# Kernel tuning notes

Hardware: AMD Instinct MI355X
Metric: run time of the kernel (lower is better)

Reference implementation:

```python
import jax, jax.numpy as jnp
import numpy as np

SIM_RADIUS = 4
SIM_STRIDE = 1
IN_STRIDES = (8, 16, 32)
REL_STRIDES = tuple(IN_STRIDES[-1] // s for s in IN_STRIDES)  # (4, 2, 1)
BN_EPS = 1e-5


def _base_conv(x, w, g, b, m, v):
    # BaseConv(c, c, ksize=1): bias-free 1x1 conv + BatchNorm2d (eval stats) + SiLU
    # x: [N, Cin, H, W], w: [Cout, Cin]
    y = jnp.einsum('nchw,dc->ndhw', x, w)
    scale = g * jax.lax.rsqrt(v + BN_EPS)
    y = y * scale[None, :, None, None] + (b - m * scale)[None, :, None, None]
    return y * jax.nn.sigmoid(y)


def _interp_indices(pci, fci):
    # Exact port of interpolate_features index selection (tiny, host-side ints).
    pci = np.asarray(pci).astype(np.int64).tolist()
    fci = np.asarray(fci).astype(np.int64).tolist()
    TP = len(pci[0])
    idx = []
    for i, (p, f) in enumerate(zip(pci, fci)):
        p_pos = TP - 2
        for f_i in f:
            while p_pos >= 0:
                if p_pos == 0 or f_i < -p[p_pos - 1]:
                    idx.append(p_pos + i * TP)
                    break
                p_pos -= 1
    return np.asarray(idx, dtype=np.int64)


def _local_corr(f1, f2, radius, step):
    # Full-image correlation over a (2r+1)x(2r+1) grid of shifts with stride `step`.
    # Equivalent to F.conv2d(f1[None], f2[:, None], stride=step, padding=radius*step,
    # groups=N*C). f1, f2: [N, C, H, W] -> [N, C, (2r+1)^2]
    N, C, H, W = f1.shape
    pad = radius * step
    f1p = jnp.pad(f1, ((0, 0), (0, 0), (pad, pad), (pad, pad)))
    sims = []
    for oy in range(2 * radius + 1):
        for ox in range(2 * radius + 1):
            sl = f1p[:, :, oy * step:oy * step + H, ox * step:ox * step + W]
            sims.append(jnp.einsum('nchw,nchw->nc', sl, f2))
    return jnp.stack(sims, axis=-1)


def _forward(feats, conv_params, mlp_w, pci, fci):
    B, TP = pci.shape
    TF = fci.shape[1]
    idx = _interp_indices(pci, fci)  # [B*TF] gather indices into flattened (B*TP)
    sims = []
    for f, (w, g, b, m, v), s in zip(feats, conv_params, REL_STRIDES):
        _, _, C, H, W = f.shape
        pf = _base_conv(f.reshape(B * TP, C, H, W), w, g, b, m, v)  # [B*TP, C, H, W]
        # interpolate_features detaches -> stop_gradient on the gathered clip features
        ipf = jax.lax.stop_gradient(pf[idx])  # [B*TF, C, H, W]
        pf = pf.reshape(B, TP, C, H, W)
        f1 = jnp.broadcast_to(pf[:, -1][:, None], (B, TF, C, H, W)).reshape(B * TF, C, H, W)
        sim = _local_corr(f1, ipf, SIM_RADIUS, SIM_STRIDE * s)  # [B*TF, C, 81]
        sim = jax.nn.softmax(sim, axis=-1)
        sim = jnp.einsum('ncs,s->nc', sim, mlp_w[0])  # Linear(81, 1, bias=False)
        sims.append(sim.reshape(B, TF, C, 1, 1))
    return tuple(sims)


def setup_inputs() -> dict:
    key = jax.random.key(0)
    ks = jax.random.split(key, 20)
    B, TP, TF = 4, 4, 2
    chans = (128, 256, 512)
    hws = ((80, 80), (40, 40), (20, 20))
    d = {}
    for l, (C, (H, W)) in enumerate(zip(chans, hws)):
        d[f'features_{l}'] = jax.random.normal(ks[l], (B, TP, C, H, W), jnp.float32)
        d[f'w{l}'] = jax.random.normal(ks[3 + l], (C, C), jnp.float32) / np.float32(np.sqrt(C))
        d[f'g{l}'] = jnp.ones((C,), jnp.float32)
        d[f'b{l}'] = jnp.zeros((C,), jnp.float32)
        d[f'm{l}'] = 0.1 * jax.random.normal(ks[6 + l], (C,), jnp.float32)
        d[f'v{l}'] = jax.random.uniform(ks[9 + l], (C,), jnp.float32, 0.5, 1.5)
    d['mlp_w'] = jax.random.normal(ks[12], (1, (2 * SIM_RADIUS + 1) ** 2), jnp.float32) / np.float32(2 * SIM_RADIUS + 1)
    d['past_clip_ids'] = jnp.tile(jnp.array([-3, -2, -1, 0], jnp.int32), (B, 1))
    d['future_clip_ids'] = jnp.tile(jnp.array([1, 2], jnp.int32), (B, 1))
    return d


def reference(features_0, features_1, features_2,
              w0, g0, b0, m0, v0,
              w1, g1, b1, m1, v1,
              w2, g2, b2, m2, v2,
              mlp_w, past_clip_ids, future_clip_ids):
    feats = (features_0, features_1, features_2)
    cps = ((w0, g0, b0, m0, v0), (w1, g1, b1, m1, v1), (w2, g2, b2, m2, v2))
    return _forward(feats, cps, mlp_w, np.asarray(past_clip_ids), np.asarray(future_clip_ids))


if __name__ == '__main__':
    outs = reference(**setup_inputs())
    print([o.shape for o in outs])
```

## Files before the change

kernel.cpp:

```cpp
#include <hip/hip_runtime.h>
#include <hip/hip_bf16.h>
#include <math.h>

#define BB 4
#define TPP 4
#define TFF 2
#define NIMG (BB*TPP)
#define NF (BB*TFF)

typedef __attribute__((ext_vector_type(8))) short bf16x8;
typedef __attribute__((ext_vector_type(4))) float f32x4;
#define MFMA16(a,b,c) __builtin_amdgcn_mfma_f32_16x16x32_bf16(a,b,c,0,0,0)

#define GLL(gaddr, laddr) __builtin_amdgcn_global_load_lds( \
    (const __attribute__((address_space(1))) void*)(gaddr), \
    (__attribute__((address_space(3))) void*)(laddr), 16, 0, 0)

__device__ __forceinline__ unsigned short f2bf(float x) {
    __hip_bfloat16 h = __float2bfloat16(x);
    return *reinterpret_cast<unsigned short*>(&h);
}
__device__ __forceinline__ float bf2f(unsigned short u) {
    unsigned int v = ((unsigned int)u) << 16;
    return __uint_as_float(v);
}

__global__ void idx_kernel(const int* __restrict__ pci, const int* __restrict__ fci,
                           int* __restrict__ idx, int* __restrict__ needed)
{
    if (threadIdx.x == 0 && blockIdx.x == 0) {
        for (int n = 0; n < BB*TPP; n++) needed[n] = 0;
        for (int i = 0; i < BB; i++) {
            needed[i*TPP + TPP-1] = 1;
            int p_pos = TPP - 2;
            for (int j = 0; j < TFF; j++) {
                int f = fci[i*TFF + j];
                while (p_pos >= 0) {
                    if (p_pos == 0 || f < -pci[i*TPP + p_pos - 1]) {
                        idx[i*TFF + j] = p_pos + i*TPP;
                        needed[p_pos + i*TPP] = 1;
                        break;
                    }
                    p_pos--;
                }
            }
        }
    }
}

template<int C>
__device__ __forceinline__ void wtile_frag(const float* __restrict__ w,
                                           const float* __restrict__ g,
                                           const float* __restrict__ v,
                                           unsigned short* __restrict__ whi,
                                           unsigned short* __restrict__ wlo, int tile)
{
    constexpr int DT = C/16;
    const int ct = tile / DT, dt = tile % DT;
    const int t = threadIdx.x;
    const size_t base = (size_t)tile * 512;
    #pragma unroll
    for (int e = 0; e < 2; e++) {
        int pos = t*2 + e;
        int lane = pos >> 3, j = pos & 7;
        int m = lane & 15, q = lane >> 4;
        int d = dt*16 + m, c = ct*32 + q*8 + j;
        float sc = g[d] * rsqrtf(v[d] + 1e-5f);
        float x = w[(size_t)d*C + c] * sc;
        unsigned short hi = f2bf(x);
        float lof = x - bf2f(hi);
        whi[base + pos] = hi;
        wlo[base + pos] = f2bf(lof);
    }
}

__global__ __launch_bounds__(256)
void wprep_kernel(const float* w0, const float* g0, const float* b0, const float* m0, const float* v0,
                  unsigned short* whi0, unsigned short* wlo0, float* sh0,
                  const float* w1, const float* g1, const float* b1, const float* m1, const float* v1,
                  unsigned short* whi1, unsigned short* wlo1, float* sh1,
                  const float* w2, const float* g2, const float* b2, const float* m2, const float* v2,
                  unsigned short* whi2, unsigned short* wlo2, float* sh2)
{
    int bid = blockIdx.x;
    if (bid < 32)        wtile_frag<128>(w0, g0, v0, whi0, wlo0, bid);
    else if (bid < 160)  wtile_frag<256>(w1, g1, v1, whi1, wlo1, bid - 32);
    else if (bid < 672)  wtile_frag<512>(w2, g2, v2, whi2, wlo2, bid - 160);
    else {
        for (int i = threadIdx.x; i < 896; i += 256) {
            if (i < 128)      { int d=i;     float sc=g0[d]*rsqrtf(v0[d]+1e-5f); sh0[d]=b0[d]-m0[d]*sc; }
            else if (i < 384) { int d=i-128; float sc=g1[d]*rsqrtf(v1[d]+1e-5f); sh1[d]=b1[d]-m1[d]*sc; }
            else              { int d=i-384; float sc=g2[d]*rsqrtf(v2[d]+1e-5f); sh2[d]=b2[d]-m2[d]*sc; }
        }
    }
}

template<int C, int HW>
__device__ __forceinline__ void conv_mfma_tile(
    const float* __restrict__ x,
    const unsigned short* __restrict__ whi,
    const unsigned short* __restrict__ wlo,
    const float* __restrict__ sh,
    float* __restrict__ pf,
    int n, int dblk, int pblk,
    unsigned short* __restrict__ Ahi, unsigned short* __restrict__ Alo,
    unsigned short* __restrict__ Bhi, unsigned short* __restrict__ Blo)
{
    constexpr int DT = C/16;
    const int tid  = threadIdx.x;
    const int lane = tid & 63;
    const int wv   = tid >> 6;
    const int d0 = dblk*128, p0 = pblk*128;
    const float* xn = x + (size_t)n * C * HW;
    const int wdt = (wv >> 1) * 4;
    const int wpt = (wv & 1) * 4;
    const int kb  = (lane >> 4) * 8;
    const int pn  = lane & 15;

    f32x4 acc[4][4];
    #pragma unroll
    for (int i = 0; i < 4; i++)
        #pragma unroll
        for (int j = 0; j < 4; j++)
            acc[i][j] = f32x4{0.f, 0.f, 0.f, 0.f};

    for (int ct = 0; ct < C/32; ct++) {
        __syncthreads();
        {
            const size_t gb = ((size_t)ct * DT + dblk*8) * 512 + (size_t)lane*8;
            const unsigned short* ghi = whi + gb;
            const unsigned short* glo = wlo + gb;
            GLL(ghi + (size_t)wv*512,     Ahi + wv*512);
            GLL(ghi + (size_t)(wv+4)*512, Ahi + (wv+4)*512);
            GLL(glo + (size_t)wv*512,     Alo + wv*512);
            GLL(glo + (size_t)(wv+4)*512, Alo + (wv+4)*512);
        }
        #pragma unroll
        for (int e = 0; e < 2; e++) {
            int pt = e*4 + (tid >> 6);
            int pp = p0 + pt*16 + pn;
            int pc = pp < HW ? pp : HW-1;
            const float* src = xn + (size_t)(ct*32 + kb) * HW + pc;
            bf16x8 h8, l8;
            #pragma unroll
            for (int j = 0; j < 8; j++) {
                float xv = src[(size_t)j * HW];
                unsigned short hi = f2bf(xv);
                h8[j] = (short)hi;
                l8[j] = (short)f2bf(xv - bf2f(hi));
            }
            int slot = pt*64 + lane;
            *(bf16x8*)(Bhi + slot*8) = h8;
            *(bf16x8*)(Blo + slot*8) = l8;
        }
        __syncthreads();
        bf16x8 bh[4], bl[4];
        #pragma unroll
        for (int j = 0; j < 4; j++) {
            bh[j] = *(const bf16x8*)(Bhi + (wpt+j)*512 + lane*8);
            bl[j] = *(const bf16x8*)(Blo + (wpt+j)*512 + lane*8);
        }
        #pragma unroll
        for (int i = 0; i < 4; i++) {
            bf16x8 ah = *(const bf16x8*)(Ahi + (wdt+i)*512 + lane*8);
            bf16x8 al = *(const bf16x8*)(Alo + (wdt+i)*512 + lane*8);
            #pragma unroll
            for (int j = 0; j < 4; j++) {
                acc[i][j] = MFMA16(ah, bh[j], acc[i][j]);
                acc[i][j] = MFMA16(al, bh[j], acc[i][j]);
                acc[i][j] = MFMA16(ah, bl[j], acc[i][j]);
            }
        }
    }

    const int rowq = (lane >> 4) * 4;
    #pragma unroll
    for (int i = 0; i < 4; i++) {
        #pragma unroll
        for (int r = 0; r < 4; r++) {
            int d = d0 + (wdt+i)*16 + rowq + r;
            float shd = sh[d];
            float* dst = pf + ((size_t)n * C + d) * HW;
            #pragma unroll
            for (int j = 0; j < 4; j++) {
                int p = p0 + (wpt+j)*16 + pn;
                float y = acc[i][j][r] + shd;
                float o = y / (1.f + __expf(-y));
                if (p < HW) dst[p] = o;
            }
        }
    }
}

__global__ __launch_bounds__(256, 2)
void conv_all(const float* x0, const unsigned short* whi0, const unsigned short* wlo0,
              const float* sh0, float* pf0,
              const float* x1, const unsigned short* whi1, const unsigned short* wlo1,
              const float* sh1, float* pf1,
              const float* x2, const unsigned short* whi2, const unsigned short* wlo2,
              const float* sh2, float* pf2,
              const int* __restrict__ needed)
{
    __shared__ __align__(16) unsigned short Ahi[8*512];
    __shared__ __align__(16) unsigned short Alo[8*512];
    __shared__ __align__(16) unsigned short Bhi[8*512];
    __shared__ __align__(16) unsigned short Blo[8*512];
    const int bid = blockIdx.x;
    if (bid < 256) {
        int n = bid >> 4, d = (bid >> 2) & 3, p = bid & 3;
        if (!needed[n]) return;
        conv_mfma_tile<512, 400>(x2, whi2, wlo2, sh2, pf2, n, d, p, Ahi, Alo, Bhi, Blo);
    } else if (bid < 672) {
        int rel = bid - 256;
        int n = rel / 26, rem = rel % 26;
        int d = rem / 13, p = rem % 13;
        if (!needed[n]) return;
        conv_mfma_tile<256, 1600>(x1, whi1, wlo1, sh1, pf1, n, d, p, Ahi, Alo, Bhi, Blo);
    } else {
        int rel = bid - 672;
        int n = rel / 50, p = rel % 50;
        if (!needed[n]) return;
        conv_mfma_tile<128, 6400>(x0, whi0, wlo0, sh0, pf0, n, 0, p, Ahi, Alo, Bhi, Blo);
    }
}

#define MAXPLANE 12544

template<int C, int H, int W, int STEP>
__device__ __forceinline__ void corr_tile(const float* __restrict__ pf,
                                          const int* __restrict__ idx,
                                          const float* __restrict__ mlp,
                                          float* __restrict__ out,
                                          int c, int b, float* __restrict__ smem)
{
    constexpr int PAD  = 4 * STEP;
    constexpr int PW   = W + 2*PAD;
    constexpr int PH   = H + 2*PAD;
    constexpr int HW   = H * W;
    constexpr int QPH   = (HW/4) / 2;
    constexpr int ITERS = (QPH + 63) / 64;
    constexpr int WINF  = 8*STEP + 4;
    constexpr int WIN4  = WINF / 4;

    float* f1s  = smem;
    float* part = smem + MAXPLANE;
    float* simC = part + 324;

    const int tid  = threadIdx.x;
    const int lane = tid & 63;
    const int wave = tid >> 6;
    const int ph   = wave / 3;
    const int kys  = wave % 3;

    const float* f1  = pf + ((size_t)(b*TPP + TPP-1) * C + c) * HW;
    const float* f2a = pf + ((size_t)idx[b*TFF + 0] * C + c) * HW;
    const float* f2b = pf + ((size_t)idx[b*TFF + 1] * C + c) * HW;

    for (int i = tid; i < PH*PW; i += 384) {
        int y = i / PW - PAD;
        int x = i % PW - PAD;
        float val = 0.f;
        if (y >= 0 && y < H && x >= 0 && x < W) val = f1[y*W + x];
        f1s[i] = val;
    }
    __syncthreads();

    float acc[2][3][9];
    #pragma unroll
    for (int f = 0; f < 2; f++)
        #pragma unroll
        for (int j = 0; j < 3; j++)
            #pragma unroll
            for (int k = 0; k < 9; k++) acc[f][j][k] = 0.f;

    for (int it = 0; it < ITERS; it++) {
        int q = ph*QPH + it*64 + lane;
        if (q < (ph+1)*QPH) {
            int p4 = q * 4;
            int h  = p4 / W;
            int w0 = p4 % W;
            float4 fa = *(const float4*)(f2a + p4);
            float4 fb = *(const float4*)(f2b + p4);
            #pragma unroll
            for (int j = 0; j < 3; j++) {
                int ky = kys*3 + j;
                const float* row = &f1s[(h + PAD + (ky-4)*STEP) * PW + w0];
                float win[WINF];
                #pragma unroll
                for (int t = 0; t < WIN4; t++)
                    *(float4*)&win[t*4] = *(const float4*)&row[t*4];
                #pragma unroll
                for (int kx = 0; kx < 9; kx++) {
                    float w0v = win[kx*STEP+0], w1v = win[kx*STEP+1];
                    float w2v = win[kx*STEP+2], w3v = win[kx*STEP+3];
                    float sa = acc[0][j][kx];
                    sa = fmaf(w0v, fa.x, sa); sa = fmaf(w1v, fa.y, sa);
                    sa = fmaf(w2v, fa.z, sa); sa = fmaf(w3v, fa.w, sa);
                    acc[0][j][kx] = sa;
                    float sb = acc[1][j][kx];
                    sb = fmaf(w0v, fb.x, sb); sb = fmaf(w1v, fb.y, sb);
                    sb = fmaf(w2v, fb.z, sb); sb = fmaf(w3v, fb.w, sb);
                    acc[1][j][kx] = sb;
                }
            }
        }
    }

    #pragma unroll
    for (int f = 0; f < 2; f++)
        #pragma unroll
        for (int j = 0; j < 3; j++)
            #pragma unroll
            for (int kx = 0; kx < 9; kx++) {
                float v = acc[f][j][kx];
                v += __shfl_xor(v, 32);
                v += __shfl_xor(v, 16);
                v += __shfl_xor(v, 8);
                v += __shfl_xor(v, 4);
                v += __shfl_xor(v, 2);
                v += __shfl_xor(v, 1);
                if (lane == 0) part[(ph*2 + f)*81 + (kys*3 + j)*9 + kx] = v;
            }
    __syncthreads();
    if (tid < 162) {
        int f = tid / 81, k = tid % 81;
        simC[f*81 + k] = part[(0*2 + f)*81 + k] + part[(1*2 + f)*81 + k];
    }
    __syncthreads();

    if (tid < 128) {
        int f = wave;
        float v0 = simC[f*81 + lane];
        float v1 = (lane + 64 < 81) ? simC[f*81 + lane + 64] : -INFINITY;
        float mx = fmaxf(v0, v1);
        #pragma unroll
        for (int m = 32; m; m >>= 1) mx = fmaxf(mx, __shfl_xor(mx, m));
        float e0 = __expf(v0 - mx);
        float e1 = (lane + 64 < 81) ? __expf(v1 - mx) : 0.f;
        float ssum = e0 + e1;
        float dsum = e0 * mlp[lane] + ((lane + 64 < 81) ? e1 * mlp[lane + 64] : 0.f);
        #pragma unroll
        for (int m = 32; m; m >>= 1) {
            ssum += __shfl_xor(ssum, m);
            dsum += __shfl_xor(dsum, m);
        }
        if (lane == 0) out[(size_t)(b*TFF + f) * C + c] = dsum / ssum;
    }
}

__global__ __launch_bounds__(384)
void corr_all(const float* __restrict__ pf0, const float* __restrict__ pf1,
              const float* __restrict__ pf2, const int* __restrict__ idx,
              const float* __restrict__ mlp, float* __restrict__ out)
{
    extern __shared__ float smem[];
    const int bid = blockIdx.x;
    if (bid < 512) {
        corr_tile<128, 80, 80, 4>(pf0, idx, mlp, out, bid & 127, bid >> 7, smem);
    } else if (bid < 1536) {
        int r = bid - 512;
        corr_tile<256, 40, 40, 2>(pf1, idx, mlp, out + (size_t)NF*128, r & 255, r >> 8, smem);
    } else {
        int r = bid - 1536;
        corr_tile<512, 20, 20, 1>(pf2, idx, mlp, out + (size_t)NF*(128+256), r & 511, r >> 9, smem);
    }
}

extern "C" void kernel_launch(void* const* d_in, const int* in_sizes, int n_in,
                              void* d_out, int out_size, void* d_ws, size_t ws_size,
                              hipStream_t stream)
{
    const float* feat0 = (const float*)d_in[0];
    const float* w0 = (const float*)d_in[1];
    const float* g0 = (const float*)d_in[2];
    const float* b0 = (const float*)d_in[3];
    const float* m0 = (const float*)d_in[4];
    const float* v0 = (const float*)d_in[5];
    const float* feat1 = (const float*)d_in[6];
    const float* w1 = (const float*)d_in[7];
    const float* g1 = (const float*)d_in[8];
    const float* b1 = (const float*)d_in[9];
    const float* m1 = (const float*)d_in[10];
    const float* v1 = (const float*)d_in[11];
    const float* feat2 = (const float*)d_in[12];
    const float* w2 = (const float*)d_in[13];
    const float* g2 = (const float*)d_in[14];
    const float* b2 = (const float*)d_in[15];
    const float* m2 = (const float*)d_in[16];
    const float* v2 = (const float*)d_in[17];
    const float* mlp = (const float*)d_in[18];
    const int* pci = (const int*)d_in[19];
    const int* fci = (const int*)d_in[20];

    float* out = (float*)d_out;

    char* base = (char*)d_ws;
    int* idxp    = (int*)base;
    int* neededp = idxp + 8;
    float* sh0 = (float*)(base + 256);
    float* sh1 = sh0 + 128;
    float* sh2 = sh1 + 256;
    unsigned short* whi0 = (unsigned short*)(sh2 + 512);
    unsigned short* wlo0 = whi0 + 128*128;
    unsigned short* whi1 = wlo0 + 128*128;
    unsigned short* wlo1 = whi1 + 256*256;
    unsigned short* whi2 = wlo1 + 256*256;
    unsigned short* wlo2 = whi2 + 512*512;
    float* pf0 = (float*)(wlo2 + 512*512);
    float* pf1 = pf0 + (size_t)NIMG * 128 * 6400;
    float* pf2 = pf1 + (size_t)NIMG * 256 * 1600;

    idx_kernel<<<1, 64, 0, stream>>>(pci, fci, idxp, neededp);
    wprep_kernel<<<673, 256, 0, stream>>>(
        w0, g0, b0, m0, v0, whi0, wlo0, sh0,
        w1, g1, b1, m1, v1, whi1, wlo1, sh1,
        w2, g2, b2, m2, v2, whi2, wlo2, sh2);

    conv_all<<<1472, 256, 0, stream>>>(
        feat0, whi0, wlo0, sh0, pf0,
        feat1, whi1, wlo1, sh1, pf1,
        feat2, whi2, wlo2, sh2, pf2,
        neededp);

    corr_all<<<3584, 384, (MAXPLANE + 324 + 162) * sizeof(float), stream>>>(
        pf0, pf1, pf2, idxp, mlp, out);
}
```

Measured before the change: 432.1 us.

## Split correlation into row-chunked partial kernel plus separate softmax finalize kernel

The correlation stage is split into row chunks. Each block now loads only its chunk of the padded f1 plane plus halo, using float4 loads, into a much smaller LDS footprint. Blocks shrink to 256 threads with launch_bounds(256,4) for higher occupancy, and partial 81-tap sums go to a global workspace. A second small kernel sums the chunks and applies the softmax-weighted MLP. In exchange the halo rows are loaded redundantly, the 9 ky rows are split unevenly across 4 waves (3,2,2,2), and there is an extra launch and global round-trip.

```diff
diff --git a/kernel.cpp b/kernel.cpp
--- a/kernel.cpp
+++ b/kernel.cpp
@@ -224,44 +224,43 @@
     }
 }
 
-#define MAXPLANE 12544
-
-template<int C, int H, int W, int STEP>
-__device__ __forceinline__ void corr_tile(const float* __restrict__ pf,
-                                          const int* __restrict__ idx,
-                                          const float* __restrict__ mlp,
-                                          float* __restrict__ out,
-                                          int c, int b, float* __restrict__ smem)
+template<int C, int H, int W, int STEP, int CHUNKS>
+__device__ __forceinline__ void corr_partial_tile(
+    const float* __restrict__ pf, const int* __restrict__ idx,
+    float* __restrict__ part, int c, int b, int chunk, float* __restrict__ f1s)
 {
     constexpr int PAD  = 4 * STEP;
     constexpr int PW   = W + 2*PAD;
-    constexpr int PH   = H + 2*PAD;
     constexpr int HW   = H * W;
-    constexpr int QPH   = (HW/4) / 2;
-    constexpr int ITERS = (QPH + 63) / 64;
+    constexpr int HC   = H / CHUNKS;
+    constexpr int ROWS = HC + 2*PAD;
+    constexpr int PQ   = PW / 4;
+    constexpr int WQ   = W / 4;
+    constexpr int QUADS = HC * WQ;
+    constexpr int ITERS = (QUADS + 63) / 64;
     constexpr int WINF  = 8*STEP + 4;
     constexpr int WIN4  = WINF / 4;
-
-    float* f1s  = smem;
-    float* part = smem + MAXPLANE;
-    float* simC = part + 324;
 
     const int tid  = threadIdx.x;
     const int lane = tid & 63;
     const int wave = tid >> 6;
-    const int ph   = wave / 3;
-    const int kys  = wave % 3;
-
+    const int ky0  = (wave == 0) ? 0 : (wave*2 + 1);
+    const int nky  = (wave == 0) ? 3 : 2;
+
+    const int r0 = chunk * HC;
     const float* f1  = pf + ((size_t)(b*TPP + TPP-1) * C + c) * HW;
-    const float* f2a = pf + ((size_t)idx[b*TFF + 0] * C + c) * HW;
-    const float* f2b = pf + ((size_t)idx[b*TFF + 1] * C + c) * HW;
-
-    for (int i = tid; i < PH*PW; i += 384) {
-        int y = i / PW - PAD;
-        int x = i % PW - PAD;
-        float val = 0.f;
-        if (y >= 0 && y < H && x >= 0 && x < W) val = f1[y*W + x];
-        f1s[i] = val;
+    const float* f2a = pf + ((size_t)idx[b*TFF + 0] * C + c) * HW + (size_t)r0 * W;
+    const float* f2b = pf + ((size_t)idx[b*TFF + 1] * C + c) * HW + (size_t)r0 * W;
+
+    for (int s = tid; s < ROWS*PQ; s += 256) {
+        int lr = s / PQ;
+        int q  = s - lr*PQ;
+        int y  = r0 + lr - PAD;
+        int x4 = q*4 - PAD;
+        float4 v = make_float4(0.f, 0.f, 0.f, 0.f);
+        if (y >= 0 && y < H && x4 >= 0 && x4 < W)
+            v = *(const float4*)(f1 + (size_t)y*W + x4);
+        *(float4*)&f1s[lr*PW + q*4] = v;
     }
     __syncthreads();
 
@@ -274,95 +273,127 @@
             for (int k = 0; k < 9; k++) acc[f][j][k] = 0.f;
 
     for (int it = 0; it < ITERS; it++) {
-        int q = ph*QPH + it*64 + lane;
-        if (q < (ph+1)*QPH) {
+        int q = it*64 + lane;
+        if (q < QUADS) {
+            int hl = q / WQ;
+            int w0 = (q - hl*WQ) * 4;
             int p4 = q * 4;
-            int h  = p4 / W;
-            int w0 = p4 % W;
             float4 fa = *(const float4*)(f2a + p4);
             float4 fb = *(const float4*)(f2b + p4);
             #pragma unroll
             for (int j = 0; j < 3; j++) {
-                int ky = kys*3 + j;
-                const float* row = &f1s[(h + PAD + (ky-4)*STEP) * PW + w0];
-                float win[WINF];
-                #pragma unroll
-                for (int t = 0; t < WIN4; t++)
-                    *(float4*)&win[t*4] = *(const float4*)&row[t*4];
+                if (j < nky) {
+                    int ky = ky0 + j;
+                    const float* row = &f1s[(hl + PAD + (ky-4)*STEP) * PW + w0];
+                    float win[WINF];
+                    #pragma unroll
+                    for (int t = 0; t < WIN4; t++)
+                        *(float4*)&win[t*4] = *(const float4*)&row[t*4];
+                    #pragma unroll
+                    for (int kx = 0; kx < 9; kx++) {
+                        float w0v = win[kx*STEP+0], w1v = win[kx*STEP+1];
+                        float w2v = win[kx*STEP+2], w3v = win[kx*STEP+3];
+                        float sa = acc[0][j][kx];
+                        sa = fmaf(w0v, fa.x, sa); sa = fmaf(w1v, fa.y, sa);
+                        sa = fmaf(w2v, fa.z, sa); sa = fmaf(w3v, fa.w, sa);
+                        acc[0][j][kx] = sa;
+                        float sb = acc[1][j][kx];
+                        sb = fmaf(w0v, fb.x, sb); sb = fmaf(w1v, fb.y, sb);
+                        sb = fmaf(w2v, fb.z, sb); sb = fmaf(w3v, fb.w, sb);
+                        acc[1][j][kx] = sb;
+                    }
+                }
+            }
+        }
+    }
+
+    float* pb = part + ((((size_t)b*C + c)*CHUNKS + chunk)*2) * 81;
+    #pragma unroll
+    for (int f = 0; f < 2; f++)
+        #pragma unroll
+        for (int j = 0; j < 3; j++) {
+            if (j < nky) {
                 #pragma unroll
                 for (int kx = 0; kx < 9; kx++) {
-                    float w0v = win[kx*STEP+0], w1v = win[kx*STEP+1];
-                    float w2v = win[kx*STEP+2], w3v = win[kx*STEP+3];
-                    float sa = acc[0][j][kx];
-                    sa = fmaf(w0v, fa.x, sa); sa = fmaf(w1v, fa.y, sa);
-                    sa = fmaf(w2v, fa.z, sa); sa = fmaf(w3v, fa.w, sa);
-                    acc[0][j][kx] = sa;
-                    float sb = acc[1][j][kx];
-                    sb = fmaf(w0v, fb.x, sb); sb = fmaf(w1v, fb.y, sb);
-                    sb = fmaf(w2v, fb.z, sb); sb = fmaf(w3v, fb.w, sb);
-                    acc[1][j][kx] = sb;
+                    float v = acc[f][j][kx];
+                    v += __shfl_xor(v, 32);
+                    v += __shfl_xor(v, 16);
+                    v += __shfl_xor(v, 8);
+                    v += __shfl_xor(v, 4);
+                    v += __shfl_xor(v, 2);
+                    v += __shfl_xor(v, 1);
+                    if (lane == 0) pb[(size_t)f*81 + (ky0+j)*9 + kx] = v;
                 }
             }
         }
-    }
-
-    #pragma unroll
-    for (int f = 0; f < 2; f++)
-        #pragma unroll
-        for (int j = 0; j < 3; j++)
-            #pragma unroll
-            for (int kx = 0; kx < 9; kx++) {
-                float v = acc[f][j][kx];
-                v += __shfl_xor(v, 32);
-                v += __shfl_xor(v, 16);
-                v += __shfl_xor(v, 8);
-                v += __shfl_xor(v, 4);
-                v += __shfl_xor(v, 2);
-                v += __shfl_xor(v, 1);
-                if (lane == 0) part[(ph*2 + f)*81 + (kys*3 + j)*9 + kx] = v;
-            }
-    __syncthreads();
-    if (tid < 162) {
-        int f = tid / 81, k = tid % 81;
-        simC[f*81 + k] = part[(0*2 + f)*81 + k] + part[(1*2 + f)*81 + k];
-    }
-    __syncthreads();
-
-    if (tid < 128) {
-        int f = wave;
-        float v0 = simC[f*81 + lane];
-        float v1 = (lane + 64 < 81) ? simC[f*81 + lane + 64] : -INFINITY;
-        float mx = fmaxf(v0, v1);
-        #pragma unroll
-        for (int m = 32; m; m >>= 1) mx = fmaxf(mx, __shfl_xor(mx, m));
-        float e0 = __expf(v0 - mx);
-        float e1 = (lane + 64 < 81) ? __expf(v1 - mx) : 0.f;
-        float ssum = e0 + e1;
-        float dsum = e0 * mlp[lane] + ((lane + 64 < 81) ? e1 * mlp[lane + 64] : 0.f);
-        #pragma unroll
-        for (int m = 32; m; m >>= 1) {
-            ssum += __shfl_xor(ssum, m);
-            dsum += __shfl_xor(dsum, m);
-        }
-        if (lane == 0) out[(size_t)(b*TFF + f) * C + c] = dsum / ssum;
-    }
-}
-
-__global__ __launch_bounds__(384)
-void corr_all(const float* __restrict__ pf0, const float* __restrict__ pf1,
-              const float* __restrict__ pf2, const int* __restrict__ idx,
-              const float* __restrict__ mlp, float* __restrict__ out)
+}
+
+__global__ __launch_bounds__(256, 4)
+void corr_partial(const float* __restrict__ pf0, const float* __restrict__ pf1,
+                  const float* __restrict__ pf2, const int* __restrict__ idx,
+                  float* __restrict__ P0, float* __restrict__ P1, float* __restrict__ P2)
 {
     extern __shared__ float smem[];
     const int bid = blockIdx.x;
+    if (bid < 2048) {
+        int b = bid >> 9, c = (bid >> 2) & 127, ch = bid & 3;
+        corr_partial_tile<128, 80, 80, 4, 4>(pf0, idx, P0, c, b, ch, smem);
+    } else if (bid < 4096) {
+        int r = bid - 2048;
+        int b = r >> 9, c = (r >> 1) & 255, ch = r & 1;
+        corr_partial_tile<256, 40, 40, 2, 2>(pf1, idx, P1, c, b, ch, smem);
+    } else {
+        int r = bid - 4096;
+        int b = r >> 9, c = r & 511;
+        corr_partial_tile<512, 20, 20, 1, 1>(pf2, idx, P2, c, b, 0, smem);
+    }
+}
+
+template<int C, int CHUNKS>
+__device__ __forceinline__ void fin_tile(const float* __restrict__ part,
+                                         const float* __restrict__ mlp,
+                                         float* __restrict__ out, int b, int c)
+{
+    const int tid  = threadIdx.x;
+    const int lane = tid & 63;
+    const int f    = tid >> 6;
+    const float* p = part + ((((size_t)b*C + c)*CHUNKS)*2 + f) * 81;
+    float v0 = 0.f, v1 = 0.f;
+    #pragma unroll
+    for (int ch = 0; ch < CHUNKS; ch++) {
+        v0 += p[(size_t)ch*162 + lane];
+        if (lane + 64 < 81) v1 += p[(size_t)ch*162 + lane + 64];
+    }
+    if (lane + 64 >= 81) v1 = -INFINITY;
+    float mx = fmaxf(v0, v1);
+    #pragma unroll
+    for (int m = 32; m; m >>= 1) mx = fmaxf(mx, __shfl_xor(mx, m));
+    float e0 = __expf(v0 - mx);
+    float e1 = (lane + 64 < 81) ? __expf(v1 - mx) : 0.f;
+    float ssum = e0 + e1;
+    float dsum = e0 * mlp[lane] + ((lane + 64 < 81) ? e1 * mlp[lane + 64] : 0.f);
+    #pragma unroll
+    for (int m = 32; m; m >>= 1) {
+        ssum += __shfl_xor(ssum, m);
+        dsum += __shfl_xor(dsum, m);
+    }
+    if (lane == 0) out[(size_t)(b*TFF + f) * C + c] = dsum / ssum;
+}
+
+__global__ __launch_bounds__(128)
+void corr_fin(const float* __restrict__ P0, const float* __restrict__ P1,
+              const float* __restrict__ P2, const float* __restrict__ mlp,
+              float* __restrict__ out)
+{
+    const int bid = blockIdx.x;
     if (bid < 512) {
-        corr_tile<128, 80, 80, 4>(pf0, idx, mlp, out, bid & 127, bid >> 7, smem);
+        fin_tile<128, 4>(P0, mlp, out, bid >> 7, bid & 127);
     } else if (bid < 1536) {
         int r = bid - 512;
-        corr_tile<256, 40, 40, 2>(pf1, idx, mlp, out + (size_t)NF*128, r & 255, r >> 8, smem);
+        fin_tile<256, 2>(P1, mlp, out + (size_t)NF*128, r >> 8, r & 255);
     } else {
         int r = bid - 1536;
-        corr_tile<512, 20, 20, 1>(pf2, idx, mlp, out + (size_t)NF*(128+256), r & 511, r >> 9, smem);
+        fin_tile<512, 1>(P2, mlp, out + (size_t)NF*(128+256), r >> 9, r & 511);
     }
 }
 
@@ -409,6 +440,9 @@
     float* pf0 = (float*)(wlo2 + 512*512);
     float* pf1 = pf0 + (size_t)NIMG * 128 * 6400;
     float* pf2 = pf1 + (size_t)NIMG * 256 * 1600;
+    float* P0  = pf2 + (size_t)NIMG * 512 * 400;
+    float* P1  = P0 + (size_t)BB * 128 * 4 * 2 * 81;
+    float* P2  = P1 + (size_t)BB * 256 * 2 * 2 * 81;
 
     idx_kernel<<<1, 64, 0, stream>>>(pci, fci, idxp, neededp);
     wprep_kernel<<<673, 256, 0, stream>>>(
@@ -422,6 +456,8 @@
         feat2, whi2, wlo2, sh2, pf2,
         neededp);
 
-    corr_all<<<3584, 384, (MAXPLANE + 324 + 162) * sizeof(float), stream>>>(
-        pf0, pf1, pf2, idxp, mlp, out);
-}
+    corr_partial<<<6144, 256, 52*112*sizeof(float), stream>>>(
+        pf0, pf1, pf2, idxp, P0, P1, P2);
+
+    corr_fin<<<3584, 128, 0, stream>>>(P0, P1, P2, mlp, out);
+}
```

Result: slower. 728.0 us (+68.5%).

## Restructure correlation tile: per-wave frame split, multi-quad register windows, vectorized staging

Applied to the files above, without the earlier changes.

The correlation kernel now gives each wave group one future frame instead of splitting pixels across halves and computing both frames per wave. Each lane handles QG consecutive float4 quads per row (4 at stride 4, 2 at stride 2), so one shared-memory window load is reused across more pixels and fewer LDS reads are issued per FMA. The padded f1 plane is staged with float4 loads, and the shared partial-sum combine stage and its barrier are removed. The trade-off is more registers for the wider window and the fa[QG] array, plus a smaller shared allocation tied to the largest padded plane.

```diff
diff --git a/kernel.cpp b/kernel.cpp
--- a/kernel.cpp
+++ b/kernel.cpp
@@ -224,114 +224,108 @@
     }
 }
 
-#define MAXPLANE 12544
-
-template<int C, int H, int W, int STEP>
-__device__ __forceinline__ void corr_tile(const float* __restrict__ pf,
-                                          const int* __restrict__ idx,
-                                          const float* __restrict__ mlp,
-                                          float* __restrict__ out,
-                                          int c, int b, float* __restrict__ smem)
+template<int C, int H, int W, int STEP, int QG>
+__device__ __forceinline__ void corr_tile(
+    const float* __restrict__ pf, const int* __restrict__ idx,
+    const float* __restrict__ mlp, float* __restrict__ out,
+    int c, int b, float* __restrict__ smem)
 {
     constexpr int PAD  = 4 * STEP;
     constexpr int PW   = W + 2*PAD;
     constexpr int PH   = H + 2*PAD;
     constexpr int HW   = H * W;
-    constexpr int QPH   = (HW/4) / 2;
-    constexpr int ITERS = (QPH + 63) / 64;
-    constexpr int WINF  = 8*STEP + 4;
-    constexpr int WIN4  = WINF / 4;
+    constexpr int PQ   = PW / 4;
+    constexpr int GPR  = W / (4*QG);
+    constexpr int GROUPS = H * GPR;
+    constexpr int ITERS  = (GROUPS + 63) / 64;
+    constexpr int WINF   = 8*STEP + 4*QG;
+    constexpr int WIN4   = WINF / 4;
 
     float* f1s  = smem;
-    float* part = smem + MAXPLANE;
-    float* simC = part + 324;
+    float* part = smem + PH*PW;
 
     const int tid  = threadIdx.x;
     const int lane = tid & 63;
     const int wave = tid >> 6;
-    const int ph   = wave / 3;
+    const int fr   = wave / 3;
     const int kys  = wave % 3;
 
-    const float* f1  = pf + ((size_t)(b*TPP + TPP-1) * C + c) * HW;
-    const float* f2a = pf + ((size_t)idx[b*TFF + 0] * C + c) * HW;
-    const float* f2b = pf + ((size_t)idx[b*TFF + 1] * C + c) * HW;
-
-    for (int i = tid; i < PH*PW; i += 384) {
-        int y = i / PW - PAD;
-        int x = i % PW - PAD;
-        float val = 0.f;
-        if (y >= 0 && y < H && x >= 0 && x < W) val = f1[y*W + x];
-        f1s[i] = val;
+    const float* f1 = pf + ((size_t)(b*TPP + TPP-1) * C + c) * HW;
+    const float* f2 = pf + ((size_t)idx[b*TFF + fr] * C + c) * HW;
+
+    for (int s = tid; s < PH*PQ; s += 384) {
+        int lr = s / PQ;
+        int q  = s - lr*PQ;
+        int y  = lr - PAD;
+        int x4 = q*4 - PAD;
+        float4 v = make_float4(0.f, 0.f, 0.f, 0.f);
+        if (y >= 0 && y < H && x4 >= 0 && x4 < W)
+            v = *(const float4*)(f1 + (size_t)y*W + x4);
+        *(float4*)&f1s[lr*PW + q*4] = v;
     }
     __syncthreads();
 
-    float acc[2][3][9];
+    float acc[3][9];
     #pragma unroll
-    for (int f = 0; f < 2; f++)
-        #pragma unroll
-        for (int j = 0; j < 3; j++)
+    for (int j = 0; j < 3; j++)
+        #pragma unroll
+        for (int k = 0; k < 9; k++) acc[j][k] = 0.f;
+
+    #pragma unroll 1
+    for (int it = 0; it < ITERS; it++) {
+        int g = it*64 + lane;
+        if (g < GROUPS) {
+            int hl  = g / GPR;
+            int col = (g - hl*GPR) * (4*QG);
+            const float* src = f2 + (size_t)hl*W + col;
+            float4 fa[QG];
             #pragma unroll
-            for (int k = 0; k < 9; k++) acc[f][j][k] = 0.f;
-
-    for (int it = 0; it < ITERS; it++) {
-        int q = ph*QPH + it*64 + lane;
-        if (q < (ph+1)*QPH) {
-            int p4 = q * 4;
-            int h  = p4 / W;
-            int w0 = p4 % W;
-            float4 fa = *(const float4*)(f2a + p4);
-            float4 fb = *(const float4*)(f2b + p4);
+            for (int qi = 0; qi < QG; qi++)
+                fa[qi] = *(const float4*)(src + qi*4);
             #pragma unroll
             for (int j = 0; j < 3; j++) {
                 int ky = kys*3 + j;
-                const float* row = &f1s[(h + PAD + (ky-4)*STEP) * PW + w0];
+                const float* row = &f1s[(hl + PAD + (ky-4)*STEP) * PW + col];
                 float win[WINF];
                 #pragma unroll
                 for (int t = 0; t < WIN4; t++)
                     *(float4*)&win[t*4] = *(const float4*)&row[t*4];
                 #pragma unroll
                 for (int kx = 0; kx < 9; kx++) {
-                    float w0v = win[kx*STEP+0], w1v = win[kx*STEP+1];
-                    float w2v = win[kx*STEP+2], w3v = win[kx*STEP+3];
-                    float sa = acc[0][j][kx];
-                    sa = fmaf(w0v, fa.x, sa); sa = fmaf(w1v, fa.y, sa);
-                    sa = fmaf(w2v, fa.z, sa); sa = fmaf(w3v, fa.w, sa);
-                    acc[0][j][kx] = sa;
-                    float sb = acc[1][j][kx];
-                    sb = fmaf(w0v, fb.x, sb); sb = fmaf(w1v, fb.y, sb);
-                    sb = fmaf(w2v, fb.z, sb); sb = fmaf(w3v, fb.w, sb);
-                    acc[1][j][kx] = sb;
+                    float s = acc[j][kx];
+                    #pragma unroll
+                    for (int qi = 0; qi < QG; qi++) {
+                        const float* wp = &win[kx*STEP + qi*4];
+                        s = fmaf(wp[0], fa[qi].x, s);
+                        s = fmaf(wp[1], fa[qi].y, s);
+                        s = fmaf(wp[2], fa[qi].z, s);
+                        s = fmaf(wp[3], fa[qi].w, s);
+                    }
+                    acc[j][kx] = s;
                 }
             }
         }
     }
 
     #pragma unroll
-    for (int f = 0; f < 2; f++)
-        #pragma unroll
-        for (int j = 0; j < 3; j++)
-            #pragma unroll
-            for (int kx = 0; kx < 9; kx++) {
-                float v = acc[f][j][kx];
-                v += __shfl_xor(v, 32);
-                v += __shfl_xor(v, 16);
-                v += __shfl_xor(v, 8);
-                v += __shfl_xor(v, 4);
-                v += __shfl_xor(v, 2);
-                v += __shfl_xor(v, 1);
-                if (lane == 0) part[(ph*2 + f)*81 + (kys*3 + j)*9 + kx] = v;
-            }
-    __syncthreads();
-    if (tid < 162) {
-        int f = tid / 81, k = tid % 81;
-        simC[f*81 + k] = part[(0*2 + f)*81 + k] + part[(1*2 + f)*81 + k];
-    }
+    for (int j = 0; j < 3; j++)
+        #pragma unroll
+        for (int kx = 0; kx < 9; kx++) {
+            float v = acc[j][kx];
+            v += __shfl_xor(v, 32);
+            v += __shfl_xor(v, 16);
+            v += __shfl_xor(v, 8);
+            v += __shfl_xor(v, 4);
+            v += __shfl_xor(v, 2);
+            v += __shfl_xor(v, 1);
+            if (lane == 0) part[fr*81 + (kys*3 + j)*9 + kx] = v;
+        }
     __syncthreads();
 
     if (tid < 128) {
         int f = wave;
-        float v0 = simC[f*81 + lane];
-        float v1 = (lane + 64 < 81) ? simC[f*81 + lane + 64] : -INFINITY;
+        float v0 = part[f*81 + lane];
+        float v1 = (lane + 64 < 81) ? part[f*81 + lane + 64] : -INFINITY;
         float mx = fmaxf(v0, v1);
         #pragma unroll
         for (int m = 32; m; m >>= 1) mx = fmaxf(mx, __shfl_xor(mx, m));
@@ -356,13 +350,13 @@
     extern __shared__ float smem[];
     const int bid = blockIdx.x;
     if (bid < 512) {
-        corr_tile<128, 80, 80, 4>(pf0, idx, mlp, out, bid & 127, bid >> 7, smem);
+        corr_tile<128, 80, 80, 4, 4>(pf0, idx, mlp, out, bid & 127, bid >> 7, smem);
     } else if (bid < 1536) {
         int r = bid - 512;
-        corr_tile<256, 40, 40, 2>(pf1, idx, mlp, out + (size_t)NF*128, r & 255, r >> 8, smem);
+        corr_tile<256, 40, 40, 2, 2>(pf1, idx, mlp, out + (size_t)NF*128, r & 255, r >> 8, smem);
     } else {
         int r = bid - 1536;
-        corr_tile<512, 20, 20, 1>(pf2, idx, mlp, out + (size_t)NF*(128+256), r & 511, r >> 9, smem);
+        corr_tile<512, 20, 20, 1, 1>(pf2, idx, mlp, out + (size_t)NF*(128+256), r & 511, r >> 9, smem);
     }
 }
 
@@ -422,6 +416,6 @@
         feat2, whi2, wlo2, sh2, pf2,
         neededp);
 
-    corr_all<<<3584, 384, (MAXPLANE + 324 + 162) * sizeof(float), stream>>>(
+    corr_all<<<3584, 384, (112*112 + 176) * sizeof(float), stream>>>(
         pf0, pf1, pf2, idxp, mlp, out);
 }
```

Result: faster. 389.1 us (-10.0%).
